# Kernel optimization log

Hardware: AMD Instinct MI355X
Metric: run time of the kernel (lower is better)

## Reference

```python
import jax, jax.numpy as jnp
import numpy as np

D = 128
SCALE = 1.0 / np.sqrt(D)  # scalar_value


def setup_inputs() -> dict:
    key = jax.random.key(0)
    k1, k2, k3 = jax.random.split(key, 3)
    B, N, S = 2, 16, 2048
    q = jax.random.normal(k1, (B, N, S, D), dtype=jnp.float32)
    k = jax.random.normal(k2, (B, N, S, D), dtype=jnp.float32)
    v = jax.random.normal(k3, (B, N, S, D), dtype=jnp.float32)
    return {"q": q, "k": k, "v": v}


def reference(q, k, v):
    # BNSD layout. scores = scale * Q K^T, causal mask, softmax with
    # explicit max/sum tracking (golden for NPU fusion attention).
    s1, s2 = q.shape[2], k.shape[2]
    scores = jnp.einsum('bnsd,bntd->bnst', q, k) * SCALE
    # generate_attn_mask: causal (lower-triangular kept), masked -> -inf
    causal = jnp.triu(jnp.ones((s1, s2), dtype=bool), k=1)
    scores = jnp.where(causal, -jnp.inf, scores)
    softmax_max = jnp.max(scores, axis=-1, keepdims=True)          # [B,N,S,1]
    exp_scores = jnp.exp(scores - softmax_max)
    softmax_sum = jnp.sum(exp_scores, axis=-1, keepdims=True)      # [B,N,S,1]
    softmax_res = exp_scores / softmax_sum
    out = jnp.einsum('bnst,bntd->bnsd', softmax_res, v)
    # NPU golden repeats stats x8 along last dim
    return (out,
            jnp.tile(softmax_max, (1, 1, 1, 8)),
            jnp.tile(softmax_sum, (1, 1, 1, 8)))
```

## Files before the change

### kernel.cpp

```cpp
#include <hip/hip_runtime.h>
#include <math.h>
#include <stdint.h>

#define D_DIM 128
#define SEQ 2048
#define NHEADS 32
#define BC 64
#define SCALE 0.08838834764831843f
#define IMG_U16 24576

typedef short bf16x8 __attribute__((ext_vector_type(8)));
typedef float f32x4 __attribute__((ext_vector_type(4)));

union Frag { uint32_t u[4]; bf16x8 v; unsigned short s[8]; };
union Pack8 { unsigned short s[8]; uint4 q; };

__device__ __forceinline__ uint32_t fbits(float x) { return __builtin_bit_cast(uint32_t, x); }
__device__ __forceinline__ float bbits(uint32_t u) { return __builtin_bit_cast(float, u); }
__device__ __forceinline__ unsigned short bf16_rne(float x) {
    uint32_t u = fbits(x);
    u += 0x7FFFu + ((u >> 16) & 1u);
    return (unsigned short)(u >> 16);
}
__device__ __forceinline__ void split2(float a, float b, uint32_t& hp, uint32_t& lp) {
    uint32_t ua = fbits(a) & 0xFFFF0000u, ub = fbits(b) & 0xFFFF0000u;
    float la = a - bbits(ua), lb = b - bbits(ub);
    hp = (ua >> 16) | ub;
    lp = (fbits(la) >> 16) | (fbits(lb) & 0xFFFF0000u);
}

__device__ __forceinline__ void gl_lds16(const unsigned short* g, unsigned short* l) {
    __builtin_amdgcn_global_load_lds(
        (const __attribute__((address_space(1))) uint32_t*)g,
        (__attribute__((address_space(3))) uint32_t*)l, 16, 0, 0);
}

__global__ __launch_bounds__(256) void cvt_kv(
    const float* __restrict__ k, const float* __restrict__ v, unsigned short* __restrict__ ws)
{
    const int b = blockIdx.x;
    const int h = b >> 5, jt = b & 31;
    const int t = (int)threadIdx.x;
    unsigned short* img = ws + (size_t)b * IMG_U16;
    const float* kp = k + ((size_t)h * SEQ + jt * 64) * D_DIM;
    const float* vp = v + ((size_t)h * SEQ + jt * 64) * D_DIM;

    #pragma unroll
    for (int u = 0; u < 4; ++u) {
        int idx = u * 256 + t;
        int n = idx >> 4, kc8 = idx & 15;
        float e[8];
        *(float4*)(e)     = *(const float4*)(kp + (size_t)n * D_DIM + kc8 * 8);
        *(float4*)(e + 4) = *(const float4*)(kp + (size_t)n * D_DIM + kc8 * 8 + 4);
        uint32_t hp[4], lp[4];
        #pragma unroll
        for (int j = 0; j < 4; ++j) split2(e[2 * j], e[2 * j + 1], hp[j], lp[j]);
        int off = n * 128 + ((kc8 ^ (n & 7)) * 8);
        *(uint4*)(img + off)        = make_uint4(hp[0], hp[1], hp[2], hp[3]);
        *(uint4*)(img + 8192 + off) = make_uint4(lp[0], lp[1], lp[2], lp[3]);
    }
    #pragma unroll
    for (int u = 0; u < 4; ++u) {
        int idx = u * 256 + t;
        int d = idx >> 3, cc = idx & 7;
        Pack8 p8;
        #pragma unroll
        for (int j = 0; j < 8; ++j)
            p8.s[j] = bf16_rne(vp[(size_t)(cc * 8 + j) * D_DIM + d]);
        int off = d * 64 + ((cc ^ (d & 7)) * 8);
        *(uint4*)(img + 16384 + off) = p8.q;
    }
}

__global__ __launch_bounds__(512, 2) void fa_fwd3(
    const float* __restrict__ q, const unsigned short* __restrict__ ws, float* __restrict__ out)
{
    __shared__ __align__(16) unsigned short Stage[2][IMG_U16];
    __shared__ __align__(16) unsigned short Pbs[128 * 64];

    const int x = blockIdx.x;
    const int it = 15 - (x >> 5);
    const int h = x & 31;

    const int t    = (int)threadIdx.x;
    const int wb   = t >> 6;
    const int lane = t & 63;
    const int ln   = lane & 15;
    const int qd   = lane >> 4;

    const unsigned short* wsh = ws + (size_t)(h * 32) * IMG_U16;
    float* out_o = out;
    float* out_m = out + (size_t)NHEADS * SEQ * D_DIM;
    float* out_l = out_m + (size_t)NHEADS * SEQ * 8;

    const int qrow0 = it * 128 + wb * 16;

    {
        const unsigned short* g = wsh + wb * 3072 + lane * 8;
        unsigned short* l = &Stage[0][wb * 3072];
        #pragma unroll
        for (int i = 0; i < 6; ++i) gl_lds16(g + i * 512, l + i * 512);
    }

    Frag Qh[4], Ql[4];
    {
        const float* qp = q + ((size_t)h * SEQ + qrow0 + ln) * D_DIM;
        #pragma unroll
        for (int kc = 0; kc < 4; ++kc) {
            const int kb = kc * 32 + qd * 8;
            float e[8];
            *(float4*)(e)     = *(const float4*)(qp + kb);
            *(float4*)(e + 4) = *(const float4*)(qp + kb + 4);
            #pragma unroll
            for (int j = 0; j < 4; ++j)
                split2(e[2 * j], e[2 * j + 1], Qh[kc].u[j], Ql[kc].u[j]);
        }
    }

    f32x4 accO[8];
    float m_r[4], l_r[4];
    #pragma unroll
    for (int nd = 0; nd < 8; ++nd) accO[nd] = (f32x4){0.f, 0.f, 0.f, 0.f};
    #pragma unroll
    for (int r = 0; r < 4; ++r) { m_r[r] = -INFINITY; l_r[r] = 0.f; }

    const int jt_end = 2 * it + 1;
    for (int jt = 0; jt <= jt_end; ++jt) {
        const int c0 = jt * BC;
        __syncthreads();

        if (jt < jt_end) {
            const unsigned short* g = wsh + (size_t)(jt + 1) * IMG_U16 + wb * 3072 + lane * 8;
            unsigned short* l = &Stage[(jt + 1) & 1][wb * 3072];
            #pragma unroll
            for (int i = 0; i < 6; ++i) gl_lds16(g + i * 512, l + i * 512);
        }

        const unsigned short* Khs = Stage[jt & 1];
        const unsigned short* Kls = Khs + 8192;
        const unsigned short* Vhs = Khs + 16384;

        if (c0 <= qrow0 + 15) {
            f32x4 accS[4];
            #pragma unroll
            for (int nt = 0; nt < 4; ++nt) accS[nt] = (f32x4){0.f, 0.f, 0.f, 0.f};
            #pragma unroll
            for (int kc = 0; kc < 4; ++kc) {
                #pragma unroll
                for (int nt = 0; nt < 4; ++nt) {
                    int n = nt * 16 + ln;
                    int off = n * 128 + (((kc * 4 + qd) ^ (n & 7)) * 8);
                    Frag Bh, Bl;
                    Bh.v = *(const bf16x8*)(Khs + off);
                    Bl.v = *(const bf16x8*)(Kls + off);
                    f32x4 c = accS[nt];
                    c = __builtin_amdgcn_mfma_f32_16x16x32_bf16(Qh[kc].v, Bh.v, c, 0, 0, 0);
                    c = __builtin_amdgcn_mfma_f32_16x16x32_bf16(Qh[kc].v, Bl.v, c, 0, 0, 0);
                    c = __builtin_amdgcn_mfma_f32_16x16x32_bf16(Ql[kc].v, Bh.v, c, 0, 0, 0);
                    accS[nt] = c;
                }
            }
            #pragma unroll
            for (int r = 0; r < 4; ++r) {
                const int rowg = qrow0 + qd * 4 + r;
                float sv[4], mx = -INFINITY;
                #pragma unroll
                for (int nt = 0; nt < 4; ++nt) {
                    float s = accS[nt][r] * SCALE;
                    if (c0 + nt * 16 + ln > rowg) s = -INFINITY;
                    sv[nt] = s; mx = fmaxf(mx, s);
                }
                #pragma unroll
                for (int off = 1; off < 16; off <<= 1) mx = fmaxf(mx, __shfl_xor(mx, off));
                const float mnew = fmaxf(m_r[r], mx);
                const float alpha = __expf(m_r[r] - mnew);
                float p[4], rs = 0.f;
                #pragma unroll
                for (int nt = 0; nt < 4; ++nt) { p[nt] = __expf(sv[nt] - mnew); rs += p[nt]; }
                #pragma unroll
                for (int off = 1; off < 16; off <<= 1) rs += __shfl_xor(rs, off);
                m_r[r] = mnew;
                l_r[r] = l_r[r] * alpha + rs;
                #pragma unroll
                for (int nd = 0; nd < 8; ++nd) accO[nd][r] *= alpha;
                const int R = wb * 16 + qd * 4 + r;
                #pragma unroll
                for (int nt = 0; nt < 4; ++nt) {
                    int c = nt * 16 + ln;
                    Pbs[R * 64 + (((c >> 3) ^ (R & 7)) * 8) + (c & 7)] = bf16_rne(p[nt]);
                }
            }
            #pragma unroll
            for (int kc2 = 0; kc2 < 2; ++kc2) {
                Frag Pf;
                const int R = wb * 16 + ln;
                Pf.v = *(const bf16x8*)(Pbs + R * 64 + (((kc2 * 4 + qd) ^ (R & 7)) * 8));
                #pragma unroll
                for (int nd = 0; nd < 8; ++nd) {
                    int dcol = nd * 16 + ln;
                    int voff = dcol * 64 + (((kc2 * 4 + qd) ^ (dcol & 7)) * 8);
                    Frag Vh2;
                    Vh2.v = *(const bf16x8*)(Vhs + voff);
                    accO[nd] = __builtin_amdgcn_mfma_f32_16x16x32_bf16(Pf.v, Vh2.v, accO[nd], 0, 0, 0);
                }
            }
        }
    }

    #pragma unroll
    for (int r = 0; r < 4; ++r) {
        const int rowg = qrow0 + qd * 4 + r;
        const float invl = 1.0f / l_r[r];
        float* op = out_o + (size_t)h * SEQ * D_DIM + (size_t)rowg * D_DIM;
        #pragma unroll
        for (int nd = 0; nd < 8; ++nd) op[nd * 16 + ln] = accO[nd][r] * invl;
        if (ln < 8) {
            size_t sb = ((size_t)h * SEQ + rowg) * 8 + ln;
            out_m[sb] = m_r[r];
            out_l[sb] = l_r[r];
        }
    }
}

__global__ __launch_bounds__(256, 2) void fa_fwd_fb(
    const float* __restrict__ q, const float* __restrict__ k,
    const float* __restrict__ v, float* __restrict__ out)
{
    __shared__ __align__(16) unsigned short Khs[64 * 128];
    __shared__ __align__(16) unsigned short Kls[64 * 128];
    __shared__ __align__(16) unsigned short Vhs[128 * 64];
    __shared__ __align__(16) unsigned short Vls[128 * 64];
    __shared__ __align__(16) unsigned short Pbs[128 * 64];

    const int x = blockIdx.x;
    const int y = x >> 3;
    const int s_idx = y & 15;
    const int h = (x & 7) * 4 + (y >> 4);
    const int it = (y < 32) ? (15 - s_idx) : s_idx;

    const int t = (int)threadIdx.x;
    const int wb = t >> 6, lane = t & 63, ln = lane & 15, qd = lane >> 4;

    const float* qh = q + (size_t)h * SEQ * D_DIM;
    const float* kh = k + (size_t)h * SEQ * D_DIM;
    const float* vh = v + (size_t)h * SEQ * D_DIM;
    float* out_o = out;
    float* out_m = out + (size_t)NHEADS * SEQ * D_DIM;
    float* out_l = out_m + (size_t)NHEADS * SEQ * 8;

    const int qrow0 = it * 128 + wb * 32;

    Frag Qh[2][4], Ql[2][4];
    #pragma unroll
    for (int mt = 0; mt < 2; ++mt) {
        const float* qp = qh + (size_t)(qrow0 + mt * 16 + ln) * D_DIM;
        #pragma unroll
        for (int kc = 0; kc < 4; ++kc) {
            const int kb = kc * 32 + qd * 8;
            float e[8];
            *(float4*)(e)     = *(const float4*)(qp + kb);
            *(float4*)(e + 4) = *(const float4*)(qp + kb + 4);
            #pragma unroll
            for (int j = 0; j < 4; ++j)
                split2(e[2 * j], e[2 * j + 1], Qh[mt][kc].u[j], Ql[mt][kc].u[j]);
        }
    }

    f32x4 accO[2][8];
    float m_r[2][4], l_r[2][4];
    #pragma unroll
    for (int mt = 0; mt < 2; ++mt) {
        #pragma unroll
        for (int nd = 0; nd < 8; ++nd) accO[mt][nd] = (f32x4){0.f, 0.f, 0.f, 0.f};
        #pragma unroll
        for (int r = 0; r < 4; ++r) { m_r[mt][r] = -INFINITY; l_r[mt][r] = 0.f; }
    }

    const int jt_end = 2 * it + 1;
    for (int jt = 0; jt <= jt_end; ++jt) {
        const int c0 = jt * BC;
        __syncthreads();
        #pragma unroll
        for (int itr = 0; itr < 8; ++itr) {
            int f = itr * 256 + t;
            int row = f >> 5, d4 = f & 31;
            float e[4];
            *(float4*)e = *(const float4*)(kh + (size_t)(c0 + row) * D_DIM + d4 * 4);
            uint32_t hp[2], lp[2];
            split2(e[0], e[1], hp[0], lp[0]);
            split2(e[2], e[3], hp[1], lp[1]);
            int off = row * 128 + (((d4 >> 1) ^ (row & 7)) * 8) + (d4 & 1) * 4;
            *(uint2*)(Khs + off) = make_uint2(hp[0], hp[1]);
            *(uint2*)(Kls + off) = make_uint2(lp[0], lp[1]);
        }
        #pragma unroll
        for (int uu = 0; uu < 4; ++uu) {
            int ug = wb * 4 + uu;
            int cc = ug >> 1, dh = ug & 1;
            int d = dh * 64 + lane;
            Frag fh, fl;
            #pragma unroll
            for (int j = 0; j < 8; j += 2) {
                float a = vh[(size_t)(c0 + cc * 8 + j) * D_DIM + d];
                float b = vh[(size_t)(c0 + cc * 8 + j + 1) * D_DIM + d];
                split2(a, b, fh.u[j >> 1], fl.u[j >> 1]);
            }
            int off = d * 64 + ((cc ^ (d & 7)) * 8);
            *(bf16x8*)(Vhs + off) = fh.v;
            *(bf16x8*)(Vls + off) = fl.v;
        }
        __syncthreads();

        if (c0 <= qrow0 + 31) {
            f32x4 accS[2][4];
            #pragma unroll
            for (int mt = 0; mt < 2; ++mt)
                #pragma unroll
                for (int nt = 0; nt < 4; ++nt) accS[mt][nt] = (f32x4){0.f, 0.f, 0.f, 0.f};
            #pragma unroll
            for (int kc = 0; kc < 4; ++kc) {
                #pragma unroll
                for (int ntp = 0; ntp < 4; ntp += 2) {
                    Frag Bh[2], Bl[2];
                    #pragma unroll
                    for (int e2 = 0; e2 < 2; ++e2) {
                        int n = (ntp + e2) * 16 + ln;
                        int off = n * 128 + (((kc * 4 + qd) ^ (n & 7)) * 8);
                        Bh[e2].v = *(const bf16x8*)(Khs + off);
                        Bl[e2].v = *(const bf16x8*)(Kls + off);
                    }
                    #pragma unroll
                    for (int mt = 0; mt < 2; ++mt)
                        #pragma unroll
                        for (int e2 = 0; e2 < 2; ++e2) {
                            f32x4 c = accS[mt][ntp + e2];
                            c = __builtin_amdgcn_mfma_f32_16x16x32_bf16(Qh[mt][kc].v, Bh[e2].v, c, 0, 0, 0);
                            c = __builtin_amdgcn_mfma_f32_16x16x32_bf16(Qh[mt][kc].v, Bl[e2].v, c, 0, 0, 0);
                            c = __builtin_amdgcn_mfma_f32_16x16x32_bf16(Ql[mt][kc].v, Bh[e2].v, c, 0, 0, 0);
                            accS[mt][ntp + e2] = c;
                        }
                }
            }
            #pragma unroll
            for (int mt = 0; mt < 2; ++mt) {
                #pragma unroll
                for (int r = 0; r < 4; ++r) {
                    const int rowg = qrow0 + mt * 16 + qd * 4 + r;
                    float sv[4], mx = -INFINITY;
                    #pragma unroll
                    for (int nt = 0; nt < 4; ++nt) {
                        float s = accS[mt][nt][r] * SCALE;
                        if (c0 + nt * 16 + ln > rowg) s = -INFINITY;
                        sv[nt] = s; mx = fmaxf(mx, s);
                    }
                    #pragma unroll
                    for (int off = 1; off < 16; off <<= 1) mx = fmaxf(mx, __shfl_xor(mx, off));
                    const float mnew = fmaxf(m_r[mt][r], mx);
                    const float alpha = __expf(m_r[mt][r] - mnew);
                    float p[4], rs = 0.f;
                    #pragma unroll
                    for (int nt = 0; nt < 4; ++nt) { p[nt] = __expf(sv[nt] - mnew); rs += p[nt]; }
                    #pragma unroll
                    for (int off = 1; off < 16; off <<= 1) rs += __shfl_xor(rs, off);
                    m_r[mt][r] = mnew;
                    l_r[mt][r] = l_r[mt][r] * alpha + rs;
                    #pragma unroll
                    for (int nd = 0; nd < 8; ++nd) accO[mt][nd][r] *= alpha;
                    const int R = wb * 32 + mt * 16 + qd * 4 + r;
                    #pragma unroll
                    for (int nt = 0; nt < 4; ++nt) {
                        int c = nt * 16 + ln;
                        Pbs[R * 64 + (((c >> 3) ^ (R & 7)) * 8) + (c & 7)] = bf16_rne(p[nt]);
                    }
                }
            }
            #pragma unroll
            for (int kc2 = 0; kc2 < 2; ++kc2) {
                Frag Pf[2];
                #pragma unroll
                for (int mt = 0; mt < 2; ++mt) {
                    int R = wb * 32 + mt * 16 + ln;
                    Pf[mt].v = *(const bf16x8*)(Pbs + R * 64 + (((kc2 * 4 + qd) ^ (R & 7)) * 8));
                }
                #pragma unroll
                for (int nd = 0; nd < 8; ++nd) {
                    int dcol = nd * 16 + ln;
                    int voff = dcol * 64 + (((kc2 * 4 + qd) ^ (dcol & 7)) * 8);
                    Frag Vh2, Vl2;
                    Vh2.v = *(const bf16x8*)(Vhs + voff);
                    Vl2.v = *(const bf16x8*)(Vls + voff);
                    #pragma unroll
                    for (int mt = 0; mt < 2; ++mt) {
                        f32x4 c = accO[mt][nd];
                        c = __builtin_amdgcn_mfma_f32_16x16x32_bf16(Pf[mt].v, Vh2.v, c, 0, 0, 0);
                        c = __builtin_amdgcn_mfma_f32_16x16x32_bf16(Pf[mt].v, Vl2.v, c, 0, 0, 0);
                        accO[mt][nd] = c;
                    }
                }
            }
        }
    }

    #pragma unroll
    for (int mt = 0; mt < 2; ++mt) {
        #pragma unroll
        for (int r = 0; r < 4; ++r) {
            const int rowg = qrow0 + mt * 16 + qd * 4 + r;
            const float invl = 1.0f / l_r[mt][r];
            float* op = out_o + (size_t)h * SEQ * D_DIM + (size_t)rowg * D_DIM;
            #pragma unroll
            for (int nd = 0; nd < 8; ++nd) op[nd * 16 + ln] = accO[mt][nd][r] * invl;
            if (ln < 8) {
                size_t sb = ((size_t)h * SEQ + rowg) * 8 + ln;
                out_m[sb] = m_r[mt][r];
                out_l[sb] = l_r[mt][r];
            }
        }
    }
}

extern "C" void kernel_launch(void* const* d_in, const int* in_sizes, int n_in,
                              void* d_out, int out_size, void* d_ws, size_t ws_size,
                              hipStream_t stream) {
    const float* q = (const float*)d_in[0];
    const float* k = (const float*)d_in[1];
    const float* v = (const float*)d_in[2];
    float* out = (float*)d_out;

    const size_t need = (size_t)1024 * IMG_U16 * sizeof(unsigned short);
    if (ws_size >= need) {
        unsigned short* ws = (unsigned short*)d_ws;
        cvt_kv<<<dim3(1024), dim3(256), 0, stream>>>(k, v, ws);
        fa_fwd3<<<dim3(512), dim3(512), 0, stream>>>(q, ws, out);
    } else {
        fa_fwd_fb<<<dim3(512), dim3(256), 0, stream>>>(q, k, v, out);
    }
}
```

Baseline: 244.9 us.

## Fuse K/V bf16 conversion into attention kernel with register-prefetched K tiles

Removes the separate cvt_kv pre-pass and the workspace image. The attention kernel now reads fp32 K/V directly, splits K into hi/lo bf16 and rounds V to bf16 into LDS each tile, and prefetches the next K tile into registers. It also folds SCALE into Q, skips the causal mask on fully visible tiles, and defers the row-sum shuffle reduction to the end. The trade is an extra barrier per tile, inline conversion work, and uncoalesced strided V loads with no async LDS double buffering, in exchange for no intermediate global write and re-read.

```diff
diff --git a/kernel.cpp b/kernel.cpp
--- a/kernel.cpp
+++ b/kernel.cpp
@@ -7,7 +7,6 @@
 #define NHEADS 32
 #define BC 64
 #define SCALE 0.08838834764831843f
-#define IMG_U16 24576
 
 typedef short bf16x8 __attribute__((ext_vector_type(8)));
 typedef float f32x4 __attribute__((ext_vector_type(4)));
@@ -29,53 +28,13 @@
     lp = (fbits(la) >> 16) | (fbits(lb) & 0xFFFF0000u);
 }
 
-__device__ __forceinline__ void gl_lds16(const unsigned short* g, unsigned short* l) {
-    __builtin_amdgcn_global_load_lds(
-        (const __attribute__((address_space(1))) uint32_t*)g,
-        (__attribute__((address_space(3))) uint32_t*)l, 16, 0, 0);
-}
-
-__global__ __launch_bounds__(256) void cvt_kv(
-    const float* __restrict__ k, const float* __restrict__ v, unsigned short* __restrict__ ws)
+__global__ __launch_bounds__(512, 2) void fa_fused(
+    const float* __restrict__ q, const float* __restrict__ k,
+    const float* __restrict__ v, float* __restrict__ out)
 {
-    const int b = blockIdx.x;
-    const int h = b >> 5, jt = b & 31;
-    const int t = (int)threadIdx.x;
-    unsigned short* img = ws + (size_t)b * IMG_U16;
-    const float* kp = k + ((size_t)h * SEQ + jt * 64) * D_DIM;
-    const float* vp = v + ((size_t)h * SEQ + jt * 64) * D_DIM;
-
-    #pragma unroll
-    for (int u = 0; u < 4; ++u) {
-        int idx = u * 256 + t;
-        int n = idx >> 4, kc8 = idx & 15;
-        float e[8];
-        *(float4*)(e)     = *(const float4*)(kp + (size_t)n * D_DIM + kc8 * 8);
-        *(float4*)(e + 4) = *(const float4*)(kp + (size_t)n * D_DIM + kc8 * 8 + 4);
-        uint32_t hp[4], lp[4];
-        #pragma unroll
-        for (int j = 0; j < 4; ++j) split2(e[2 * j], e[2 * j + 1], hp[j], lp[j]);
-        int off = n * 128 + ((kc8 ^ (n & 7)) * 8);
-        *(uint4*)(img + off)        = make_uint4(hp[0], hp[1], hp[2], hp[3]);
-        *(uint4*)(img + 8192 + off) = make_uint4(lp[0], lp[1], lp[2], lp[3]);
-    }
-    #pragma unroll
-    for (int u = 0; u < 4; ++u) {
-        int idx = u * 256 + t;
-        int d = idx >> 3, cc = idx & 7;
-        Pack8 p8;
-        #pragma unroll
-        for (int j = 0; j < 8; ++j)
-            p8.s[j] = bf16_rne(vp[(size_t)(cc * 8 + j) * D_DIM + d]);
-        int off = d * 64 + ((cc ^ (d & 7)) * 8);
-        *(uint4*)(img + 16384 + off) = p8.q;
-    }
-}
-
-__global__ __launch_bounds__(512, 2) void fa_fwd3(
-    const float* __restrict__ q, const unsigned short* __restrict__ ws, float* __restrict__ out)
-{
-    __shared__ __align__(16) unsigned short Stage[2][IMG_U16];
+    __shared__ __align__(16) unsigned short Khs[64 * 128];
+    __shared__ __align__(16) unsigned short Kls[64 * 128];
+    __shared__ __align__(16) unsigned short Vhs[128 * 64];
     __shared__ __align__(16) unsigned short Pbs[128 * 64];
 
     const int x = blockIdx.x;
@@ -88,23 +47,21 @@
     const int ln   = lane & 15;
     const int qd   = lane >> 4;
 
-    const unsigned short* wsh = ws + (size_t)(h * 32) * IMG_U16;
+    const float* qh = q + (size_t)h * SEQ * D_DIM;
+    const float* kh = k + (size_t)h * SEQ * D_DIM;
+    const float* vh = v + (size_t)h * SEQ * D_DIM;
     float* out_o = out;
     float* out_m = out + (size_t)NHEADS * SEQ * D_DIM;
     float* out_l = out_m + (size_t)NHEADS * SEQ * 8;
 
     const int qrow0 = it * 128 + wb * 16;
 
-    {
-        const unsigned short* g = wsh + wb * 3072 + lane * 8;
-        unsigned short* l = &Stage[0][wb * 3072];
-        #pragma unroll
-        for (int i = 0; i < 6; ++i) gl_lds16(g + i * 512, l + i * 512);
-    }
+    const int krow0 = t >> 5;
+    const int kd4   = t & 31;
 
     Frag Qh[4], Ql[4];
     {
-        const float* qp = q + ((size_t)h * SEQ + qrow0 + ln) * D_DIM;
+        const float* qp = qh + (size_t)(qrow0 + ln) * D_DIM;
         #pragma unroll
         for (int kc = 0; kc < 4; ++kc) {
             const int kb = kc * 32 + qd * 8;
@@ -112,10 +69,17 @@
             *(float4*)(e)     = *(const float4*)(qp + kb);
             *(float4*)(e + 4) = *(const float4*)(qp + kb + 4);
             #pragma unroll
+            for (int j = 0; j < 8; ++j) e[j] *= SCALE;
+            #pragma unroll
             for (int j = 0; j < 4; ++j)
                 split2(e[2 * j], e[2 * j + 1], Qh[kc].u[j], Ql[kc].u[j]);
         }
     }
+
+    float4 kreg[4];
+    #pragma unroll
+    for (int itr = 0; itr < 4; ++itr)
+        kreg[itr] = *(const float4*)(kh + (size_t)(itr * 16 + krow0) * D_DIM + kd4 * 4);
 
     f32x4 accO[8];
     float m_r[4], l_r[4];
@@ -127,18 +91,48 @@
     const int jt_end = 2 * it + 1;
     for (int jt = 0; jt <= jt_end; ++jt) {
         const int c0 = jt * BC;
+
         __syncthreads();
 
+        float vreg[2][8];
+        #pragma unroll
+        for (int uu = 0; uu < 2; ++uu) {
+            const int ug = wb * 2 + uu;
+            const int cc = ug >> 1;
+            const int d  = (ug & 1) * 64 + lane;
+            #pragma unroll
+            for (int j = 0; j < 8; ++j)
+                vreg[uu][j] = vh[(size_t)(c0 + cc * 8 + j) * D_DIM + d];
+        }
+        #pragma unroll
+        for (int itr = 0; itr < 4; ++itr) {
+            const int row = itr * 16 + krow0;
+            uint32_t hp0, lp0, hp1, lp1;
+            split2(kreg[itr].x, kreg[itr].y, hp0, lp0);
+            split2(kreg[itr].z, kreg[itr].w, hp1, lp1);
+            const int off = row * 128 + (((kd4 >> 1) ^ (row & 7)) * 8) + (kd4 & 1) * 4;
+            *(uint2*)(Khs + off) = make_uint2(hp0, hp1);
+            *(uint2*)(Kls + off) = make_uint2(lp0, lp1);
+        }
+        #pragma unroll
+        for (int uu = 0; uu < 2; ++uu) {
+            const int ug = wb * 2 + uu;
+            const int cc = ug >> 1;
+            const int d  = (ug & 1) * 64 + lane;
+            Pack8 p8;
+            #pragma unroll
+            for (int j = 0; j < 8; ++j) p8.s[j] = bf16_rne(vreg[uu][j]);
+            *(uint4*)(Vhs + d * 64 + ((cc ^ (d & 7)) * 8)) = p8.q;
+        }
+
+        __syncthreads();
+
         if (jt < jt_end) {
-            const unsigned short* g = wsh + (size_t)(jt + 1) * IMG_U16 + wb * 3072 + lane * 8;
-            unsigned short* l = &Stage[(jt + 1) & 1][wb * 3072];
-            #pragma unroll
-            for (int i = 0; i < 6; ++i) gl_lds16(g + i * 512, l + i * 512);
-        }
-
-        const unsigned short* Khs = Stage[jt & 1];
-        const unsigned short* Kls = Khs + 8192;
-        const unsigned short* Vhs = Khs + 16384;
+            const float* kp2 = kh + (size_t)(c0 + BC) * D_DIM;
+            #pragma unroll
+            for (int itr = 0; itr < 4; ++itr)
+                kreg[itr] = *(const float4*)(kp2 + (size_t)(itr * 16 + krow0) * D_DIM + kd4 * 4);
+        }
 
         if (c0 <= qrow0 + 15) {
             f32x4 accS[4];
@@ -160,27 +154,26 @@
                     accS[nt] = c;
                 }
             }
+            const bool needMask = (c0 + 63 > qrow0);
             #pragma unroll
             for (int r = 0; r < 4; ++r) {
                 const int rowg = qrow0 + qd * 4 + r;
                 float sv[4], mx = -INFINITY;
                 #pragma unroll
                 for (int nt = 0; nt < 4; ++nt) {
-                    float s = accS[nt][r] * SCALE;
-                    if (c0 + nt * 16 + ln > rowg) s = -INFINITY;
+                    float s = accS[nt][r];
+                    if (needMask && (c0 + nt * 16 + ln > rowg)) s = -INFINITY;
                     sv[nt] = s; mx = fmaxf(mx, s);
                 }
                 #pragma unroll
                 for (int off = 1; off < 16; off <<= 1) mx = fmaxf(mx, __shfl_xor(mx, off));
                 const float mnew = fmaxf(m_r[r], mx);
                 const float alpha = __expf(m_r[r] - mnew);
-                float p[4], rs = 0.f;
-                #pragma unroll
-                for (int nt = 0; nt < 4; ++nt) { p[nt] = __expf(sv[nt] - mnew); rs += p[nt]; }
-                #pragma unroll
-                for (int off = 1; off < 16; off <<= 1) rs += __shfl_xor(rs, off);
+                float p[4];
+                #pragma unroll
+                for (int nt = 0; nt < 4; ++nt) p[nt] = __expf(sv[nt] - mnew);
                 m_r[r] = mnew;
-                l_r[r] = l_r[r] * alpha + rs;
+                l_r[r] = l_r[r] * alpha + ((p[0] + p[1]) + (p[2] + p[3]));
                 #pragma unroll
                 for (int nd = 0; nd < 8; ++nd) accO[nd][r] *= alpha;
                 const int R = wb * 16 + qd * 4 + r;
@@ -209,6 +202,11 @@
 
     #pragma unroll
     for (int r = 0; r < 4; ++r) {
+        #pragma unroll
+        for (int off = 1; off < 16; off <<= 1) l_r[r] += __shfl_xor(l_r[r], off);
+    }
+    #pragma unroll
+    for (int r = 0; r < 4; ++r) {
         const int rowg = qrow0 + qd * 4 + r;
         const float invl = 1.0f / l_r[r];
         float* op = out_o + (size_t)h * SEQ * D_DIM + (size_t)rowg * D_DIM;
@@ -218,203 +216,6 @@
             size_t sb = ((size_t)h * SEQ + rowg) * 8 + ln;
             out_m[sb] = m_r[r];
             out_l[sb] = l_r[r];
-        }
-    }
-}
-
-__global__ __launch_bounds__(256, 2) void fa_fwd_fb(
-    const float* __restrict__ q, const float* __restrict__ k,
-    const float* __restrict__ v, float* __restrict__ out)
-{
-    __shared__ __align__(16) unsigned short Khs[64 * 128];
-    __shared__ __align__(16) unsigned short Kls[64 * 128];
-    __shared__ __align__(16) unsigned short Vhs[128 * 64];
-    __shared__ __align__(16) unsigned short Vls[128 * 64];
-    __shared__ __align__(16) unsigned short Pbs[128 * 64];
-
-    const int x = blockIdx.x;
-    const int y = x >> 3;
-    const int s_idx = y & 15;
-    const int h = (x & 7) * 4 + (y >> 4);
-    const int it = (y < 32) ? (15 - s_idx) : s_idx;
-
-    const int t = (int)threadIdx.x;
-    const int wb = t >> 6, lane = t & 63, ln = lane & 15, qd = lane >> 4;
-
-    const float* qh = q + (size_t)h * SEQ * D_DIM;
-    const float* kh = k + (size_t)h * SEQ * D_DIM;
-    const float* vh = v + (size_t)h * SEQ * D_DIM;
-    float* out_o = out;
-    float* out_m = out + (size_t)NHEADS * SEQ * D_DIM;
-    float* out_l = out_m + (size_t)NHEADS * SEQ * 8;
-
-    const int qrow0 = it * 128 + wb * 32;
-
-    Frag Qh[2][4], Ql[2][4];
-    #pragma unroll
-    for (int mt = 0; mt < 2; ++mt) {
-        const float* qp = qh + (size_t)(qrow0 + mt * 16 + ln) * D_DIM;
-        #pragma unroll
-        for (int kc = 0; kc < 4; ++kc) {
-            const int kb = kc * 32 + qd * 8;
-            float e[8];
-            *(float4*)(e)     = *(const float4*)(qp + kb);
-            *(float4*)(e + 4) = *(const float4*)(qp + kb + 4);
-            #pragma unroll
-            for (int j = 0; j < 4; ++j)
-                split2(e[2 * j], e[2 * j + 1], Qh[mt][kc].u[j], Ql[mt][kc].u[j]);
-        }
-    }
-
-    f32x4 accO[2][8];
-    float m_r[2][4], l_r[2][4];
-    #pragma unroll
-    for (int mt = 0; mt < 2; ++mt) {
-        #pragma unroll
-        for (int nd = 0; nd < 8; ++nd) accO[mt][nd] = (f32x4){0.f, 0.f, 0.f, 0.f};
-        #pragma unroll
-        for (int r = 0; r < 4; ++r) { m_r[mt][r] = -INFINITY; l_r[mt][r] = 0.f; }
-    }
-
-    const int jt_end = 2 * it + 1;
-    for (int jt = 0; jt <= jt_end; ++jt) {
-        const int c0 = jt * BC;
-        __syncthreads();
-        #pragma unroll
-        for (int itr = 0; itr < 8; ++itr) {
-            int f = itr * 256 + t;
-            int row = f >> 5, d4 = f & 31;
-            float e[4];
-            *(float4*)e = *(const float4*)(kh + (size_t)(c0 + row) * D_DIM + d4 * 4);
-            uint32_t hp[2], lp[2];
-            split2(e[0], e[1], hp[0], lp[0]);
-            split2(e[2], e[3], hp[1], lp[1]);
-            int off = row * 128 + (((d4 >> 1) ^ (row & 7)) * 8) + (d4 & 1) * 4;
-            *(uint2*)(Khs + off) = make_uint2(hp[0], hp[1]);
-            *(uint2*)(Kls + off) = make_uint2(lp[0], lp[1]);
-        }
-        #pragma unroll
-        for (int uu = 0; uu < 4; ++uu) {
-            int ug = wb * 4 + uu;
-            int cc = ug >> 1, dh = ug & 1;
-            int d = dh * 64 + lane;
-            Frag fh, fl;
-            #pragma unroll
-            for (int j = 0; j < 8; j += 2) {
-                float a = vh[(size_t)(c0 + cc * 8 + j) * D_DIM + d];
-                float b = vh[(size_t)(c0 + cc * 8 + j + 1) * D_DIM + d];
-                split2(a, b, fh.u[j >> 1], fl.u[j >> 1]);
-            }
-            int off = d * 64 + ((cc ^ (d & 7)) * 8);
-            *(bf16x8*)(Vhs + off) = fh.v;
-            *(bf16x8*)(Vls + off) = fl.v;
-        }
-        __syncthreads();
-
-        if (c0 <= qrow0 + 31) {
-            f32x4 accS[2][4];
-            #pragma unroll
-            for (int mt = 0; mt < 2; ++mt)
-                #pragma unroll
-                for (int nt = 0; nt < 4; ++nt) accS[mt][nt] = (f32x4){0.f, 0.f, 0.f, 0.f};
-            #pragma unroll
-            for (int kc = 0; kc < 4; ++kc) {
-                #pragma unroll
-                for (int ntp = 0; ntp < 4; ntp += 2) {
-                    Frag Bh[2], Bl[2];
-                    #pragma unroll
-                    for (int e2 = 0; e2 < 2; ++e2) {
-                        int n = (ntp + e2) * 16 + ln;
-                        int off = n * 128 + (((kc * 4 + qd) ^ (n & 7)) * 8);
-                        Bh[e2].v = *(const bf16x8*)(Khs + off);
-                        Bl[e2].v = *(const bf16x8*)(Kls + off);
-                    }
-                    #pragma unroll
-                    for (int mt = 0; mt < 2; ++mt)
-                        #pragma unroll
-                        for (int e2 = 0; e2 < 2; ++e2) {
-                            f32x4 c = accS[mt][ntp + e2];
-                            c = __builtin_amdgcn_mfma_f32_16x16x32_bf16(Qh[mt][kc].v, Bh[e2].v, c, 0, 0, 0);
-                            c = __builtin_amdgcn_mfma_f32_16x16x32_bf16(Qh[mt][kc].v, Bl[e2].v, c, 0, 0, 0);
-                            c = __builtin_amdgcn_mfma_f32_16x16x32_bf16(Ql[mt][kc].v, Bh[e2].v, c, 0, 0, 0);
-                            accS[mt][ntp + e2] = c;
-                        }
-                }
-            }
-            #pragma unroll
-            for (int mt = 0; mt < 2; ++mt) {
-                #pragma unroll
-                for (int r = 0; r < 4; ++r) {
-                    const int rowg = qrow0 + mt * 16 + qd * 4 + r;
-                    float sv[4], mx = -INFINITY;
-                    #pragma unroll
-                    for (int nt = 0; nt < 4; ++nt) {
-                        float s = accS[mt][nt][r] * SCALE;
-                        if (c0 + nt * 16 + ln > rowg) s = -INFINITY;
-                        sv[nt] = s; mx = fmaxf(mx, s);
-                    }
-                    #pragma unroll
-                    for (int off = 1; off < 16; off <<= 1) mx = fmaxf(mx, __shfl_xor(mx, off));
-                    const float mnew = fmaxf(m_r[mt][r], mx);
-                    const float alpha = __expf(m_r[mt][r] - mnew);
-                    float p[4], rs = 0.f;
-                    #pragma unroll
-                    for (int nt = 0; nt < 4; ++nt) { p[nt] = __expf(sv[nt] - mnew); rs += p[nt]; }
-                    #pragma unroll
-                    for (int off = 1; off < 16; off <<= 1) rs += __shfl_xor(rs, off);
-                    m_r[mt][r] = mnew;
-                    l_r[mt][r] = l_r[mt][r] * alpha + rs;
-                    #pragma unroll
-                    for (int nd = 0; nd < 8; ++nd) accO[mt][nd][r] *= alpha;
-                    const int R = wb * 32 + mt * 16 + qd * 4 + r;
-                    #pragma unroll
-                    for (int nt = 0; nt < 4; ++nt) {
-                        int c = nt * 16 + ln;
-                        Pbs[R * 64 + (((c >> 3) ^ (R & 7)) * 8) + (c & 7)] = bf16_rne(p[nt]);
-                    }
-                }
-            }
-            #pragma unroll
-            for (int kc2 = 0; kc2 < 2; ++kc2) {
-                Frag Pf[2];
-                #pragma unroll
-                for (int mt = 0; mt < 2; ++mt) {
-                    int R = wb * 32 + mt * 16 + ln;
-                    Pf[mt].v = *(const bf16x8*)(Pbs + R * 64 + (((kc2 * 4 + qd) ^ (R & 7)) * 8));
-                }
-                #pragma unroll
-                for (int nd = 0; nd < 8; ++nd) {
-                    int dcol = nd * 16 + ln;
-                    int voff = dcol * 64 + (((kc2 * 4 + qd) ^ (dcol & 7)) * 8);
-                    Frag Vh2, Vl2;
-                    Vh2.v = *(const bf16x8*)(Vhs + voff);
-                    Vl2.v = *(const bf16x8*)(Vls + voff);
-                    #pragma unroll
-                    for (int mt = 0; mt < 2; ++mt) {
-                        f32x4 c = accO[mt][nd];
-                        c = __builtin_amdgcn_mfma_f32_16x16x32_bf16(Pf[mt].v, Vh2.v, c, 0, 0, 0);
-                        c = __builtin_amdgcn_mfma_f32_16x16x32_bf16(Pf[mt].v, Vl2.v, c, 0, 0, 0);
-                        accO[mt][nd] = c;
-                    }
-                }
-            }
-        }
-    }
-
-    #pragma unroll
-    for (int mt = 0; mt < 2; ++mt) {
-        #pragma unroll
-        for (int r = 0; r < 4; ++r) {
-            const int rowg = qrow0 + mt * 16 + qd * 4 + r;
-            const float invl = 1.0f / l_r[mt][r];
-            float* op = out_o + (size_t)h * SEQ * D_DIM + (size_t)rowg * D_DIM;
-            #pragma unroll
-            for (int nd = 0; nd < 8; ++nd) op[nd * 16 + ln] = accO[mt][nd][r] * invl;
-            if (ln < 8) {
-                size_t sb = ((size_t)h * SEQ + rowg) * 8 + ln;
-                out_m[sb] = m_r[mt][r];
-                out_l[sb] = l_r[mt][r];
-            }
         }
     }
 }
@@ -426,13 +227,7 @@
     const float* k = (const float*)d_in[1];
     const float* v = (const float*)d_in[2];
     float* out = (float*)d_out;
-
-    const size_t need = (size_t)1024 * IMG_U16 * sizeof(unsigned short);
-    if (ws_size >= need) {
-        unsigned short* ws = (unsigned short*)d_ws;
-        cvt_kv<<<dim3(1024), dim3(256), 0, stream>>>(k, v, ws);
-        fa_fwd3<<<dim3(512), dim3(512), 0, stream>>>(q, ws, out);
-    } else {
-        fa_fwd_fb<<<dim3(512), dim3(256), 0, stream>>>(q, k, v, out);
-    }
-}
+    (void)d_ws; (void)ws_size;
+
+    fa_fused<<<dim3(512), dim3(512), 0, stream>>>(q, k, v, out);
+}
```

Result: no change. 244.6 us (-0.1%).
